# Kernel tuning notes

Hardware: AMD Instinct MI355X
Metric: run time of the kernel (lower is better)

## Reference

```python
import jax, jax.numpy as jnp
import numpy as np

B, T, D, F, E, K, L, S = 8, 1024, 512, 1024, 8, 2, 2, 64
SE, SH = 64, 128  # subject_embed_dim, style_hidden_dim


def setup_inputs() -> dict:
    key = jax.random.key(0)
    ks = jax.random.split(key, 16)
    r = lambda i, shape, s=0.05: (jax.random.normal(ks[i], shape, jnp.float32) * s)
    return dict(
        x=jax.random.normal(ks[0], (B, T, D), jnp.float32),
        subject_ids=jax.random.randint(ks[1], (B,), 0, S),
        # per-layer LayerNorm params (L, D)
        ln_g=jnp.ones((L, D), jnp.float32), ln_b=jnp.zeros((L, D), jnp.float32),
        # per-layer SubjectStyleAlignment params (weights stored (in, out))
        subj_emb=r(2, (L, S, SE), 0.02),
        h1_w=r(3, (L, SE, SH)), h1_b=jnp.zeros((L, SH), jnp.float32),
        h2_w=r(4, (L, SH, SH)), h2_b=jnp.zeros((L, SH), jnp.float32),
        s1_w=r(5, (L, SH, SH // 2)), s1_b=jnp.zeros((L, SH // 2), jnp.float32),
        s2_w=r(6, (L, SH // 2, 2 * D)), s2_b=jnp.zeros((L, 2 * D), jnp.float32),
        # shared TopKRouter: Linear(D, D//2) -> ReLU -> Linear(D//2, E)
        g1_w=r(7, (D, D // 2)), g1_b=jnp.zeros((D // 2,), jnp.float32),
        g2_w=r(8, (D // 2, E)), g2_b=jnp.zeros((E,), jnp.float32),
        # shared ExpertPool of GLU experts (no bias)
        wi0=r(9, (E, D, F)), wi1=r(10, (E, D, F)), wo=r(11, (E, F, D)),
    )


def _layernorm(x, g, b):
    m = x.mean(-1, keepdims=True)
    v = x.var(-1, keepdims=True)  # biased, matches torch LayerNorm
    return (x - m) / jnp.sqrt(v + 1e-5) * g + b


def reference(x, subject_ids, ln_g, ln_b, subj_emb, h1_w, h1_b, h2_w, h2_b,
              s1_w, s1_b, s2_w, s2_b, g1_w, g1_b, g2_w, g2_b, wi0, wi1, wo):
    Bs, Ts, Ds = x.shape
    for l in range(L):  # small fixed layer loop; expert pool + router are shared
        res = x
        h = _layernorm(x, ln_g[l], ln_b[l])
        # SubjectStyleAlignment: instance norm over time axis per (B, D) channel
        mu = h.mean(1, keepdims=True)
        var = h.var(1, keepdims=True)
        hn = (h - mu) / jnp.sqrt(var + 1e-8)
        e = subj_emb[l][subject_ids]                               # (B, SE)
        hh = jax.nn.relu(e @ h1_w[l] + h1_b[l]) @ h2_w[l] + h2_b[l]
        sp = jax.nn.relu(hh @ s1_w[l] + s1_b[l]) @ s2_w[l] + s2_b[l]  # (B, 2D)
        gamma = jax.nn.softplus(sp[:, :Ds]) + 1e-8
        beta = sp[:, Ds:]
        h = hn * gamma[:, None, :] + beta[:, None, :]
        # Router (shared across layers)
        hf = h.reshape(-1, Ds)                                     # (N, D)
        logits = jax.nn.relu(hf @ g1_w + g1_b) @ g2_w + g2_b       # (N, E)
        probs = jax.nn.softmax(logits, -1)
        gates, idx = jax.lax.top_k(probs, K)                       # (N, K)
        gates = gates / (gates.sum(-1, keepdims=True) + 1e-8)
        # combine weights: cw[n, e] = sum_k gates[n,k] * [idx[n,k]==e]
        cw = (jax.nn.one_hot(idx, E, dtype=hf.dtype) * gates[..., None]).sum(1)  # (N, E)
        # GLU experts, computed dense over E then gated-combined
        hid = jax.nn.relu(jnp.einsum('nd,edf->enf', hf, wi0)) \
              * jnp.einsum('nd,edf->enf', hf, wi1)                 # (E, N, F)
        eo = jnp.einsum('enf,efd->end', hid, wo)                   # (E, N, D)
        y = jnp.einsum('ne,end->nd', cw, eo)                       # (N, D)
        x = res + y.reshape(Bs, Ts, Ds)
    return x
```

## Files before the change

kernel.cpp:

```cpp
#include <hip/hip_runtime.h>

typedef unsigned short u16;
typedef unsigned int   u32;
typedef _Float16       f16;
typedef __attribute__((ext_vector_type(8))) _Float16 f16x8;
typedef __attribute__((ext_vector_type(4))) float    f32x4;
typedef __attribute__((ext_vector_type(4))) double   dbl4;

#define NSLOT_ 16384

__device__ __forceinline__ u16 f16bits(f16 h){ union{f16 f; u16 u;} x; x.f = h; return x.u; }

__device__ __forceinline__ void gl_lds16(const void* gptr, void* lptr){
  __builtin_amdgcn_global_load_lds((const __attribute__((address_space(1))) u32*)gptr,
                                   (__attribute__((address_space(3))) u32*)lptr, 16, 0, 0);
}

__device__ __forceinline__ int roff(int row, int lks){
  return ((row >> 1) << 6) + ((lks ^ ((row >> 1) & 3)) << 4) + ((row & 1) << 3);
}

__global__ __launch_bounds__(256) void ln_kernel(const float* __restrict__ x,
    const float* __restrict__ g, const float* __restrict__ bb, float* __restrict__ h){
  int n = blockIdx.x, t = threadIdx.x;
  const float* xr = x + ((size_t)n << 9);
  float2 v = *(const float2*)&xr[t*2];
  double vx = v.x, vy = v.y;
  double s = vx + vy;
  double q = vx*vx + vy*vy;
  #pragma unroll
  for (int o = 32; o > 0; o >>= 1){ s += __shfl_down(s, o, 64); q += __shfl_down(q, o, 64); }
  __shared__ double ls[4], lq_[4];
  __shared__ double sm, sv;
  int wid = t >> 6, lane = t & 63;
  if (lane == 0){ ls[wid] = s; lq_[wid] = q; }
  __syncthreads();
  if (t == 0){
    double S = ls[0]+ls[1]+ls[2]+ls[3], Q = lq_[0]+lq_[1]+lq_[2]+lq_[3];
    double mean = S * (1.0/512.0);
    double var  = Q * (1.0/512.0) - mean*mean;
    sm = mean; sv = 1.0/sqrt(var + 1e-5);
  }
  __syncthreads();
  double mean = sm, inv = sv;
  int d = t*2;
  float2 o;
  o.x = (float)((vx - mean)*inv*(double)g[d]   + (double)bb[d]);
  o.y = (float)((vy - mean)*inv*(double)g[d+1] + (double)bb[d+1]);
  *(float2*)&h[((size_t)n<<9) + d] = o;
}

__global__ __launch_bounds__(256) void colstats(const float* __restrict__ h,
    double* __restrict__ cs, double* __restrict__ cq){
  int bid = blockIdx.x;
  int b = bid >> 3, ch = bid & 7;
  int t = threadIdx.x;
  int col = ch*64 + (t & 63);
  int tp = t >> 6;
  const float* base = h + ((size_t)b << 19);
  double s = 0.0, q = 0.0;
  for (int tt = tp; tt < 1024; tt += 4){
    double v = (double)base[((size_t)tt << 9) + col];
    s += v; q += v*v;
  }
  __shared__ double ls[4][64], lq[4][64];
  ls[tp][t & 63] = s; lq[tp][t & 63] = q;
  __syncthreads();
  if (tp == 0){
    double S = ls[0][t]+ls[1][t]+ls[2][t]+ls[3][t];
    double Q = lq[0][t]+lq[1][t]+lq[2][t]+lq[3][t];
    cs[(b<<9)+col] = S; cq[(b<<9)+col] = Q;
  }
}

__global__ __launch_bounds__(256) void subj_kernel(const int* __restrict__ sid,
    const float* __restrict__ semb,
    const float* __restrict__ h1w, const float* __restrict__ h1b,
    const float* __restrict__ h2w, const float* __restrict__ h2b,
    const float* __restrict__ s1w, const float* __restrict__ s1b,
    const float* __restrict__ s2w, const float* __restrict__ s2b,
    const double* __restrict__ cs, const double* __restrict__ cq,
    double* __restrict__ a64, double* __restrict__ c64, int l){
  __shared__ double ev[64], hid1[128], hh[128], sh[64], sp[1024];
  int t = threadIdx.x;
  int b = blockIdx.x;
  int s = sid[b];
  if (t < 64) ev[t] = (double)semb[l*4096 + s*64 + t];
  __syncthreads();
  if (t < 128){
    double acc = (double)h1b[l*128 + t];
    for (int i = 0; i < 64; ++i) acc += ev[i]*(double)h1w[l*8192 + i*128 + t];
    hid1[t] = acc > 0.0 ? acc : 0.0;
  }
  __syncthreads();
  if (t < 128){
    double acc = (double)h2b[l*128 + t];
    for (int i = 0; i < 128; ++i) acc += hid1[i]*(double)h2w[l*16384 + i*128 + t];
    hh[t] = acc;
  }
  __syncthreads();
  if (t < 64){
    double acc = (double)s1b[l*64 + t];
    for (int i = 0; i < 128; ++i) acc += hh[i]*(double)s1w[l*8192 + i*64 + t];
    sh[t] = acc > 0.0 ? acc : 0.0;
  }
  __syncthreads();
  for (int m = t; m < 1024; m += 256){
    double acc = (double)s2b[l*1024 + m];
    for (int j = 0; j < 64; ++j) acc += sh[j]*(double)s2w[l*65536 + j*1024 + m];
    sp[m] = acc;
  }
  __syncthreads();
  for (int d = t; d < 512; d += 256){
    double mu  = cs[(b<<9)+d] * (1.0/1024.0);
    double var = cq[(b<<9)+d] * (1.0/1024.0) - mu*mu;
    double inv = 1.0/sqrt(var + 1e-8);
    double spv = sp[d];
    double gamma = (spv > 30.0 ? spv : log1p(exp(spv))) + 1e-8;
    double beta  = sp[512 + d];
    double A = gamma * inv;
    a64[(b<<9)+d] = A;
    c64[(b<<9)+d] = beta - mu*A;
  }
}

__global__ __launch_bounds__(256) void hfcast(const float* __restrict__ h,
    const double* __restrict__ a64, const double* __restrict__ c64,
    u16* __restrict__ hfh, u16* __restrict__ hfl){
  size_t i0 = ((size_t)blockIdx.x*256 + threadIdx.x) * 8;
  int n = (int)(i0 >> 9);
  int d0 = (int)(i0 & 511);
  int b = n >> 10;
// ... 109 lines not shown
    #pragma unroll
    for (int e = 0; e < 8; ++e){
      double v = l0[e];
      if (v > b1){ b2 = b1; i2 = i1; b1 = v; i1 = e; }
      else if (v > b2){ b2 = v; i2 = e; }
    }
    double pr1 = p[i1]/s, pr2 = p[i2]/s;
    double den = pr1 + pr2 + 1e-8;
    int n = tok0 + t;
    idxo[2*n] = i1; idxo[2*n+1] = i2;
    wo_[2*n] = (float)(pr1/den); wo_[2*n+1] = (float)(pr2/den);
    atomicAdd(&lcnt[i1], 1); atomicAdd(&lcnt[i2], 1);
  }
  __syncthreads();
  if (t < 8) atomicAdd(&counts[t], lcnt[t]);
}

__global__ void offsets_kernel(const int* __restrict__ counts, int* __restrict__ offs,
                               int* __restrict__ cur){
  if (threadIdx.x == 0 && blockIdx.x == 0){
    int run = 0;
    for (int e = 0; e < 8; ++e){ offs[e] = run; run += counts[e]; cur[e] = 0; }
  }
}

__global__ __launch_bounds__(256) void scatter_kernel(const int* __restrict__ idx,
    const int* __restrict__ offs, int* __restrict__ cur,
    int* __restrict__ tok_of, int* __restrict__ slot_of){
  __shared__ int lcnt[8], lbase[8];
  int t = threadIdx.x;
  int n = blockIdx.x*256 + t;
  if (t < 8) lcnt[t] = 0;
  __syncthreads();
  int e0 = idx[2*n], e1 = idx[2*n+1];
  int p0 = atomicAdd(&lcnt[e0], 1);
  int p1 = atomicAdd(&lcnt[e1], 1);
  __syncthreads();
  if (t < 8) lbase[t] = atomicAdd(&cur[t], lcnt[t]);
  __syncthreads();
  int s0 = offs[e0] + lbase[e0] + p0;
  int s1 = offs[e1] + lbase[e1] + p1;
  tok_of[s0] = n; tok_of[s1] = n;
  slot_of[2*n] = s0; slot_of[2*n+1] = s1;
}

__global__ __launch_bounds__(256) void cvtT16(const float* __restrict__ src,
    u16* __restrict__ dh, u16* __restrict__ dl, int R, int C){
  int bx = blockIdx.x;
  int tilesC = C >> 5, tilesR = R >> 5;
  int e = bx / (tilesR*tilesC);
  int rem = bx % (tilesR*tilesC);
  int rt = rem / tilesC, ct = rem % tilesC;
  __shared__ float tile[32][33];
  int t = threadIdx.x;
  int j = t & 31, i0 = t >> 5;
  const float* s = src + (size_t)e*R*C + (size_t)(rt*32)*C + ct*32;
  for (int ii = i0; ii < 32; ii += 8) tile[ii][j] = s[(size_t)ii*C + j];
  __syncthreads();
  size_t ob = (size_t)e*R*C + (size_t)(ct*32)*R + rt*32;
  for (int ii = i0; ii < 32; ii += 8){
    float v = tile[j][ii];
    f16 hi = (f16)v;
    float rem2 = (v - (float)hi) * 2048.f;
    f16 lo = (f16)rem2;
    dh[ob + (size_t)ii*R + j] = f16bits(hi);
    dl[ob + (size_t)ii*R + j] = f16bits(lo);
  }
}

__global__ __launch_bounds__(256) void up1_kernel(const u16* __restrict__ hfh,
    const u16* __restrict__ hfl,
    const u16* __restrict__ w0h, const u16* __restrict__ w0l,
    const u16* __restrict__ w1h, const u16* __restrict__ w1l,
    const int* __restrict__ tok_of, const int* __restrict__ offs, const int* __restrict__ counts,
    u16* __restrict__ hidh, u16* __restrict__ hidl){
  int bx = blockIdx.x;
  int e  = bx >> 11;
  int mt = (bx >> 4) & 127;
  int nt = bx & 15;
  int base = offs[e], cnt = counts[e];
  int row0 = mt << 7;
  if (row0 >= cnt) return;
  __shared__ __align__(16) u16 Ah[2][4096], Alo[2][4096];
  __shared__ __align__(16) u16 B0h[2][2048], B0l[2][2048], B1h[2][2048], B1l[2][2048];
  int t = threadIdx.x, w = t >> 6, l = t & 63;
  int wm = w >> 1, wn = w & 1;
  int lr = l & 15, lks = l >> 4;
  int riw = ((l >> 3) << 1) | (l & 1);
  int kc16s = ((((l >> 1) & 3) ^ ((l >> 3) & 3)) << 3);
  int ar1 = w*16 + riw;
  int tokA1, tokA2;
  { int ss = base + row0 + ar1;      ss = ss < NSLOT_ ? ss : NSLOT_-1; tokA1 = tok_of[ss]; }
  { int ss = base + row0 + 64 + ar1; ss = ss < NSLOT_ ? ss : NSLOT_-1; tokA2 = tok_of[ss]; }
  const u16* sAh1 = hfh + ((size_t)tokA1 << 9) + kc16s;
  const u16* sAh2 = hfh + ((size_t)tokA2 << 9) + kc16s;
  const u16* sAl1 = hfl + ((size_t)tokA1 << 9) + kc16s;
  const u16* sAl2 = hfl + ((size_t)tokA2 << 9) + kc16s;
  size_t bcol = (size_t)(e*1024 + nt*64);
  size_t bci = (bcol + (size_t)ar1) << 9;
  const u16* sB0h = w0h + bci + kc16s;
  const u16* sB0l = w0l + bci + kc16s;
  const u16* sB1h = w1h + bci + kc16s;
  const u16* sB1l = w1l + bci + kc16s;
  int aoff[4], boff[2];
  #pragma unroll
  for (int mi = 0; mi < 4; ++mi) aoff[mi] = roff(wm*64 + mi*16 + lr, lks);
  #pragma unroll
  for (int ni = 0; ni < 2; ++ni) boff[ni] = roff(wn*32 + ni*16 + lr, lks);
  f32x4 hh0[4][2], cr0[4][2], hh1[4][2], cr1[4][2];
  #pragma unroll
  for (int i = 0; i < 4; ++i)
    #pragma unroll
    for (int j = 0; j < 2; ++j)
      #pragma unroll
      for (int r = 0; r < 4; ++r){ hh0[i][j][r]=0.f; cr0[i][j][r]=0.f; hh1[i][j][r]=0.f; cr1[i][j][r]=0.f; }
#define STG_U(buf, kc) do{ \
    gl_lds16(sAh1 + (kc), &Ah[buf][t*8]); \
    gl_lds16(sAh2 + (kc), &Ah[buf][2048 + t*8]); \
    gl_lds16(sAl1 + (kc), &Alo[buf][t*8]); \
    gl_lds16(sAl2 + (kc), &Alo[buf][2048 + t*8]); \
    gl_lds16(sB0h + (kc), &B0h[buf][t*8]); \
    gl_lds16(sB0l + (kc), &B0l[buf][t*8]); \
    gl_lds16(sB1h + (kc), &B1h[buf][t*8]); \
    gl_lds16(sB1l + (kc), &B1l[buf][t*8]); }while(0)
  STG_U(0, 0);
  for (int ks = 0; ks < 16; ++ks){
    int cur = ks & 1;
    __syncthreads();
    if (ks < 15) STG_U(cur^1, (ks+1)*32);
    f16x8 ah[4], al[4], b0hv[2], b0lv[2], b1hv[2], b1lv[2];
    #pragma unroll
    for (int mi = 0; mi < 4; ++mi){
      ah[mi] = *(const f16x8*)&Ah[cur][aoff[mi]];
      al[mi] = *(const f16x8*)&Alo[cur][aoff[mi]];
    }
    #pragma unroll
    for (int ni = 0; ni < 2; ++ni){
      b0hv[ni] = *(const f16x8*)&B0h[cur][boff[ni]];
      b0lv[ni] = *(const f16x8*)&B0l[cur][boff[ni]];
      b1hv[ni] = *(const f16x8*)&B1h[cur][boff[ni]];
      b1lv[ni] = *(const f16x8*)&B1l[cur][boff[ni]];
    }
    #pragma unroll
    for (int mi = 0; mi < 4; ++mi)
      #pragma unroll
      for (int ni = 0; ni < 2; ++ni){
        hh0[mi][ni] = __builtin_amdgcn_mfma_f32_16x16x32_f16(ah[mi], b0hv[ni], hh0[mi][ni], 0, 0, 0);
        hh1[mi][ni] = __builtin_amdgcn_mfma_f32_16x16x32_f16(ah[mi], b1hv[ni], hh1[mi][ni], 0, 0, 0);
        cr0[mi][ni] = __builtin_amdgcn_mfma_f32_16x16x32_f16(ah[mi], b0lv[ni], cr0[mi][ni], 0, 0, 0);
        cr0[mi][ni] = __builtin_amdgcn_mfma_f32_16x16x32_f16(al[mi], b0hv[ni], cr0[mi][ni], 0, 0, 0);
        cr1[mi][ni] = __builtin_amdgcn_mfma_f32_16x16x32_f16(ah[mi], b1lv[ni], cr1[mi][ni], 0, 0, 0);
        cr1[mi][ni] = __builtin_amdgcn_mfma_f32_16x16x32_f16(al[mi], b1hv[ni], cr1[mi][ni], 0, 0, 0);
      }
  }
#undef STG_U
  #pragma unroll
  for (int mi = 0; mi < 4; ++mi){
    int rb = row0 + wm*64 + mi*16 + lks*4;
    #pragma unroll
    for (int r = 0; r < 4; ++r){
      int rr = rb + r;
      if (rr < cnt){
        size_t orow = ((size_t)(base + rr) << 10) + nt*64;
        #pragma unroll
        for (int ni = 0; ni < 2; ++ni){
          int col = wn*32 + ni*16 + lr;
          float u0 = hh0[mi][ni][r] + cr0[mi][ni][r]*(1.f/2048.f);
          float u1 = hh1[mi][ni][r] + cr1[mi][ni][r]*(1.f/2048.f);
          u0 = u0 > 0.f ? u0 : 0.f;
          float v = u0*u1;
          f16 vh = (f16)v;
          float rem = (v - (float)vh)*2048.f;
          hidh[orow + col] = f16bits(vh);
          hidl[orow + col] = f16bits((f16)rem);
        }
      }
    }
  }
}

__global__ __launch_bounds__(256) void down1_kernel(const u16* __restrict__ hidh,
    const u16* __restrict__ hidl, const u16* __restrict__ wdh, const u16* __restrict__ wdl,
    const int* __restrict__ offs, const int* __restrict__ counts, float* __restrict__ eo){
  int bx = blockIdx.x;
  int e  = bx >> 10;
  int mt = (bx >> 3) & 127;
  int nt = bx & 7;
  int base = offs[e], cnt = counts[e];
  int row0 = mt << 7;
  if (row0 >= cnt) return;
  __shared__ __align__(16) u16 Ah[2][4096], Alo[2][4096];
  __shared__ __align__(16) u16 Bh[2][2048], Bl[2][2048];
  int t = threadIdx.x, w = t >> 6, l = t & 63;
  int wm = w >> 1, wn = w & 1;
  int lr = l & 15, lks = l >> 4;
  int riw = ((l >> 3) << 1) | (l & 1);
  int kc16s = ((((l >> 1) & 3) ^ ((l >> 3) & 3)) << 3);
  int ar1 = w*16 + riw;
  int sA1c = base + row0 + ar1;      sA1c = sA1c < NSLOT_ ? sA1c : NSLOT_-1;
  int sA2c = base + row0 + 64 + ar1; sA2c = sA2c < NSLOT_ ? sA2c : NSLOT_-1;
  const u16* sAh1 = hidh + ((size_t)sA1c << 10) + kc16s;
  const u16* sAh2 = hidh + ((size_t)sA2c << 10) + kc16s;
  const u16* sAl1 = hidl + ((size_t)sA1c << 10) + kc16s;
  const u16* sAl2 = hidl + ((size_t)sA2c << 10) + kc16s;
  size_t bcol = (size_t)(e*512 + nt*64);
  size_t bci = (bcol + (size_t)ar1) << 10;
  const u16* sBh = wdh + bci + kc16s;
  const u16* sBl = wdl + bci + kc16s;
  int aoff[4], boff[2];
  #pragma unroll
  for (int mi = 0; mi < 4; ++mi) aoff[mi] = roff(wm*64 + mi*16 + lr, lks);
  #pragma unroll
  for (int ni = 0; ni < 2; ++ni) boff[ni] = roff(wn*32 + ni*16 + lr, lks);
  f32x4 hh[4][2], cr[4][2];
  #pragma unroll
  for (int i = 0; i < 4; ++i)
    #pragma unroll
    for (int j = 0; j < 2; ++j)
      #pragma unroll
      for (int r = 0; r < 4; ++r){ hh[i][j][r]=0.f; cr[i][j][r]=0.f; }
#define STG_D(buf, kc) do{ \
    gl_lds16(sAh1 + (kc), &Ah[buf][t*8]); \
    gl_lds16(sAh2 + (kc), &Ah[buf][2048 + t*8]); \
    gl_lds16(sAl1 + (kc), &Alo[buf][t*8]); \
    gl_lds16(sAl2 + (kc), &Alo[buf][2048 + t*8]); \
    gl_lds16(sBh + (kc), &Bh[buf][t*8]); \
    gl_lds16(sBl + (kc), &Bl[buf][t*8]); }while(0)
  STG_D(0, 0);
  for (int ks = 0; ks < 32; ++ks){
    int cur = ks & 1;
    __syncthreads();
    if (ks < 31) STG_D(cur^1, (ks+1)*32);
    f16x8 ah[4], al[4], bh[2], bl[2];
    #pragma unroll
    for (int mi = 0; mi < 4; ++mi){
      ah[mi] = *(const f16x8*)&Ah[cur][aoff[mi]];
      al[mi] = *(const f16x8*)&Alo[cur][aoff[mi]];
    }
    #pragma unroll
    for (int ni = 0; ni < 2; ++ni){
      bh[ni] = *(const f16x8*)&Bh[cur][boff[ni]];
      bl[ni] = *(const f16x8*)&Bl[cur][boff[ni]];
    }
    #pragma unroll
    for (int mi = 0; mi < 4; ++mi)
      #pragma unroll
      for (int ni = 0; ni < 2; ++ni){
        hh[mi][ni] = __builtin_amdgcn_mfma_f32_16x16x32_f16(ah[mi], bh[ni], hh[mi][ni], 0, 0, 0);
        cr[mi][ni] = __builtin_amdgcn_mfma_f32_16x16x32_f16(ah[mi], bl[ni], cr[mi][ni], 0, 0, 0);
        cr[mi][ni] = __builtin_amdgcn_mfma_f32_16x16x32_f16(al[mi], bh[ni], cr[mi][ni], 0, 0, 0);
      }
  }
#undef STG_D
  #pragma unroll
  for (int mi = 0; mi < 4; ++mi){
    int rb = row0 + wm*64 + mi*16 + lks*4;
    #pragma unroll
    for (int r = 0; r < 4; ++r){
      int rr = rb + r;
      if (rr < cnt){
        float* orow = eo + (((size_t)(base + rr)) << 9) + nt*64;
        #pragma unroll
        for (int ni = 0; ni < 2; ++ni)
          orow[wn*32 + ni*16 + lr] = hh[mi][ni][r] + cr[mi][ni][r]*(1.f/2048.f);
      }
    }
  }
}

__global__ __launch_bounds__(256) void uph_kernel(const u16* __restrict__ hfh,
    const u16* __restrict__ w0h, const u16* __restrict__ w1h,
    const int* __restrict__ tok_of, const int* __restrict__ offs, const int* __restrict__ counts,
    u16* __restrict__ hidh){
  int bx = blockIdx.x;
  int e  = bx >> 11;
  int mt = (bx >> 4) & 127;
  int nt = bx & 15;
  int base = offs[e], cnt = counts[e];
  int row0 = mt << 7;
  if (row0 >= cnt) return;
  __shared__ __align__(16) u16 Ah[2][4096];
  __shared__ __align__(16) u16 B0h[2][2048], B1h[2][2048];
  int t = threadIdx.x, w = t >> 6, l = t & 63;
  int wm = w >> 1, wn = w & 1;
  int lr = l & 15, lks = l >> 4;
  int riw = ((l >> 3) << 1) | (l & 1);
  int kc16s = ((((l >> 1) & 3) ^ ((l >> 3) & 3)) << 3);
  int ar1 = w*16 + riw;
  int tokA1, tokA2;
  { int ss = base + row0 + ar1;      ss = ss < NSLOT_ ? ss : NSLOT_-1; tokA1 = tok_of[ss]; }
  { int ss = base + row0 + 64 + ar1; ss = ss < NSLOT_ ? ss : NSLOT_-1; tokA2 = tok_of[ss]; }
  const u16* sAh1 = hfh + ((size_t)tokA1 << 9) + kc16s;
  const u16* sAh2 = hfh + ((size_t)tokA2 << 9) + kc16s;
  size_t bcol = (size_t)(e*1024 + nt*64);
  size_t bci = (bcol + (size_t)ar1) << 9;
  const u16* sB0 = w0h + bci + kc16s;
  const u16* sB1 = w1h + bci + kc16s;
  int aoff[4], boff[2];
  #pragma unroll
  for (int mi = 0; mi < 4; ++mi) aoff[mi] = roff(wm*64 + mi*16 + lr, lks);
  #pragma unroll
  for (int ni = 0; ni < 2; ++ni) boff[ni] = roff(wn*32 + ni*16 + lr, lks);
  f32x4 hh0[4][2], hh1[4][2];
  #pragma unroll
  for (int i = 0; i < 4; ++i)
    #pragma unroll
    for (int j = 0; j < 2; ++j)
      #pragma unroll
      for (int r = 0; r < 4; ++r){ hh0[i][j][r]=0.f; hh1[i][j][r]=0.f; }
#define STG_UH(buf, kc) do{ \
    gl_lds16(sAh1 + (kc), &Ah[buf][t*8]); \
    gl_lds16(sAh2 + (kc), &Ah[buf][2048 + t*8]); \
    gl_lds16(sB0 + (kc), &B0h[buf][t*8]); \
    gl_lds16(sB1 + (kc), &B1h[buf][t*8]); }while(0)
  STG_UH(0, 0);
  for (int ks = 0; ks < 16; ++ks){
    int cur = ks & 1;
    __syncthreads();
    if (ks < 15) STG_UH(cur^1, (ks+1)*32);
    f16x8 ah[4], b0v[2], b1v[2];
    #pragma unroll
    for (int mi = 0; mi < 4; ++mi) ah[mi] = *(const f16x8*)&Ah[cur][aoff[mi]];
    #pragma unroll
    for (int ni = 0; ni < 2; ++ni){
      b0v[ni] = *(const f16x8*)&B0h[cur][boff[ni]];
      b1v[ni] = *(const f16x8*)&B1h[cur][boff[ni]];
    }
    #pragma unroll
    for (int mi = 0; mi < 4; ++mi)
      #pragma unroll
      for (int ni = 0; ni < 2; ++ni){
        hh0[mi][ni] = __builtin_amdgcn_mfma_f32_16x16x32_f16(ah[mi], b0v[ni], hh0[mi][ni], 0, 0, 0);
        hh1[mi][ni] = __builtin_amdgcn_mfma_f32_16x16x32_f16(ah[mi], b1v[ni], hh1[mi][ni], 0, 0, 0);
      }
  }
#undef STG_UH
  #pragma unroll
  for (int mi = 0; mi < 4; ++mi){
    int rb = row0 + wm*64 + mi*16 + lks*4;
    #pragma unroll
    for (int r = 0; r < 4; ++r){
      int rr = rb + r;
      if (rr < cnt){
        size_t orow = ((size_t)(base + rr) << 10) + nt*64;
        #pragma unroll
        for (int ni = 0; ni < 2; ++ni){
          int col = wn*32 + ni*16 + lr;
          float u0 = hh0[mi][ni][r];
          u0 = u0 > 0.f ? u0 : 0.f;
          hidh[orow + col] = f16bits((f16)(u0*hh1[mi][ni][r]));
        }
      }
    }
  }
}

__global__ __launch_bounds__(256) void dnh_kernel(const u16* __restrict__ hidh,
    const u16* __restrict__ wdh,
    const int* __restrict__ offs, const int* __restrict__ counts, float* __restrict__ eo){
  int bx = blockIdx.x;
  int e  = bx >> 10;
  int mt = (bx >> 3) & 127;
  int nt = bx & 7;
  int base = offs[e], cnt = counts[e];
  int row0 = mt << 7;
  if (row0 >= cnt) return;
  __shared__ __align__(16) u16 Ah[2][4096];
  __shared__ __align__(16) u16 Bh[2][2048];
  int t = threadIdx.x, w = t >> 6, l = t & 63;
  int wm = w >> 1, wn = w & 1;
  int lr = l & 15, lks = l >> 4;
  int riw = ((l >> 3) << 1) | (l & 1);
  int kc16s = ((((l >> 1) & 3) ^ ((l >> 3) & 3)) << 3);
  int ar1 = w*16 + riw;
  int sA1c = base + row0 + ar1;      sA1c = sA1c < NSLOT_ ? sA1c : NSLOT_-1;
  int sA2c = base + row0 + 64 + ar1; sA2c = sA2c < NSLOT_ ? sA2c : NSLOT_-1;
  const u16* sAh1 = hidh + ((size_t)sA1c << 10) + kc16s;
  const u16* sAh2 = hidh + ((size_t)sA2c << 10) + kc16s;
  size_t bcol = (size_t)(e*512 + nt*64);
  const u16* sB = wdh + ((bcol + (size_t)ar1) << 10) + kc16s;
  int aoff[4], boff[2];
  #pragma unroll
  for (int mi = 0; mi < 4; ++mi) aoff[mi] = roff(wm*64 + mi*16 + lr, lks);
  #pragma unroll
  for (int ni = 0; ni < 2; ++ni) boff[ni] = roff(wn*32 + ni*16 + lr, lks);
  f32x4 hh[4][2];
  #pragma unroll
  for (int i = 0; i < 4; ++i)
    #pragma unroll
    for (int j = 0; j < 2; ++j)
      #pragma unroll
      for (int r = 0; r < 4; ++r) hh[i][j][r] = 0.f;
#define STG_DH(buf, kc) do{ \
    gl_lds16(sAh1 + (kc), &Ah[buf][t*8]); \
    gl_lds16(sAh2 + (kc), &Ah[buf][2048 + t*8]); \
    gl_lds16(sB + (kc), &Bh[buf][t*8]); }while(0)
  STG_DH(0, 0);
  for (int ks = 0; ks < 32; ++ks){
    int cur = ks & 1;
    __syncthreads();
    if (ks < 31) STG_DH(cur^1, (ks+1)*32);
    f16x8 ah[4], bh[2];
    #pragma unroll
    for (int mi = 0; mi < 4; ++mi) ah[mi] = *(const f16x8*)&Ah[cur][aoff[mi]];
    #pragma unroll
    for (int ni = 0; ni < 2; ++ni) bh[ni] = *(const f16x8*)&Bh[cur][boff[ni]];
    #pragma unroll
    for (int mi = 0; mi < 4; ++mi)
      #pragma unroll
      for (int ni = 0; ni < 2; ++ni)
        hh[mi][ni] = __builtin_amdgcn_mfma_f32_16x16x32_f16(ah[mi], bh[ni], hh[mi][ni], 0, 0, 0);
  }
#undef STG_DH
  #pragma unroll
  for (int mi = 0; mi < 4; ++mi){
    int rb = row0 + wm*64 + mi*16 + lks*4;
    #pragma unroll
    for (int r = 0; r < 4; ++r){
      int rr = rb + r;
      if (rr < cnt){
        float* orow = eo + (((size_t)(base + rr)) << 9) + nt*64;
        #pragma unroll
        for (int ni = 0; ni < 2; ++ni)
          orow[wn*32 + ni*16 + lr] = hh[mi][ni][r];
      }
    }
  }
}

__global__ __launch_bounds__(128) void gather_kernel(const float* __restrict__ xin,
    const float* __restrict__ eo, const int* __restrict__ slot_of, const float* __restrict__ wv,
    float* __restrict__ out){
  int n = blockIdx.x, t = threadIdx.x;
  int s0 = slot_of[2*n], s1 = slot_of[2*n+1];
  double w0 = wv[2*n], w1 = wv[2*n+1];
  float4 xi = *(const float4*)&xin[((size_t)n << 9) + t*4];
  float4 e0 = *(const float4*)&eo[((size_t)s0 << 9) + t*4];
  float4 e1 = *(const float4*)&eo[((size_t)s1 << 9) + t*4];
  float4 o;
  o.x = (float)((double)xi.x + w0*(double)e0.x + w1*(double)e1.x);
  o.y = (float)((double)xi.y + w0*(double)e0.y + w1*(double)e1.y);
  o.z = (float)((double)xi.z + w0*(double)e0.z + w1*(double)e1.z);
  o.w = (float)((double)xi.w + w0*(double)e0.w + w1*(double)e1.w);
  *(float4*)&out[((size_t)n << 9) + t*4] = o;
}

extern "C" void kernel_launch(void* const* d_in, const int* in_sizes, int n_in,
                              void* d_out, int out_size, void* d_ws, size_t ws_size,
                              hipStream_t stream) {
  (void)in_sizes; (void)n_in; (void)out_size; (void)ws_size;
  const float* x0   = (const float*)d_in[0];
  const int*   sid  = (const int*)  d_in[1];
  const float* ln_g = (const float*)d_in[2];
  const float* ln_b = (const float*)d_in[3];
  const float* semb = (const float*)d_in[4];
  const float* h1w  = (const float*)d_in[5];
  const float* h1b  = (const float*)d_in[6];
  const float* h2w  = (const float*)d_in[7];
  const float* h2b  = (const float*)d_in[8];
  const float* s1w  = (const float*)d_in[9];
  const float* s1b  = (const float*)d_in[10];
  const float* s2w  = (const float*)d_in[11];
  const float* s2b  = (const float*)d_in[12];
  const float* g1w  = (const float*)d_in[13];
  const float* g1b  = (const float*)d_in[14];
  const float* g2w  = (const float*)d_in[15];
  const float* g2b  = (const float*)d_in[16];
  const float* wi0  = (const float*)d_in[17];
  const float* wi1  = (const float*)d_in[18];
  const float* wo   = (const float*)d_in[19];

  char* W = (char*)d_ws;
  float*  h      = (float*)(W + 0);
  u16*    hfh    = (u16*)  (W + 16777216ULL);
  u16*    hfl    = (u16*)  (W + 25165824ULL);
  float*  eo32   = (float*)(W + 0);
  u16*    hid16h = (u16*)  (W + 33554432ULL);
  u16*    hid16l = (u16*)  (W + 67108864ULL);
  u16*    w0Th   = (u16*)  (W + 100663296ULL);
  u16*    w0Tl   = (u16*)  (W + 109051904ULL);
  u16*    w1Th   = (u16*)  (W + 117440512ULL);
  u16*    w1Tl   = (u16*)  (W + 125829120ULL);
  u16*    woTh   = (u16*)  (W + 134217728ULL);
  u16*    woTl   = (u16*)  (W + 142606336ULL);
  u16*    g1Th   = (u16*)  (W + 150994944ULL);
  u16*    g1Tl   = (u16*)  (W + 151257088ULL);
  double* cs     = (double*)(W + 151519232ULL);
  double* cq     = (double*)(W + 151552000ULL);
  double* a64    = (double*)(W + 151584768ULL);
  double* c64    = (double*)(W + 151617536ULL);
  int*    idxa   = (int*)   (W + 151650304ULL);
  float*  warr   = (float*) (W + 151715840ULL);
  int*    tok_of = (int*)   (W + 151781376ULL);
  int*    slot_of= (int*)   (W + 151846912ULL);
  int*    counts = (int*)   (W + 151912448ULL);
  int*    cur    = counts + 8;
  int*    offs   = counts + 16;

  cvtT16<<<4096, 256, 0, stream>>>(wi0, w0Th, w0Tl, 512, 1024);
  cvtT16<<<4096, 256, 0, stream>>>(wi1, w1Th, w1Tl, 512, 1024);
  cvtT16<<<4096, 256, 0, stream>>>(wo,  woTh, woTl, 1024, 512);
  cvtT16<<<128,  256, 0, stream>>>(g1w, g1Th, g1Tl, 512, 256);

  for (int l = 0; l < 2; ++l){
    const float* xin = l ? (const float*)d_out : x0;
    ln_kernel<<<8192, 256, 0, stream>>>(xin, ln_g + l*512, ln_b + l*512, h);
    colstats<<<64, 256, 0, stream>>>(h, cs, cq);
    subj_kernel<<<8, 256, 0, stream>>>(sid, semb, h1w, h1b, h2w, h2b, s1w, s1b, s2w, s2b,
                                       cs, cq, a64, c64, l);
    hfcast<<<2048, 256, 0, stream>>>(h, a64, c64, hfh, hfl);
    zero_counts<<<1, 64, 0, stream>>>(counts);
    gate2_kernel<<<512, 256, 0, stream>>>(hfh, hfl, g1Th, g1Tl, g1b, g2w, g2b, idxa, warr, counts);
    offsets_kernel<<<1, 1, 0, stream>>>(counts, offs, cur);
    scatter_kernel<<<32, 256, 0, stream>>>(idxa, offs, cur, tok_of, slot_of);
    if (l == 0){
      up1_kernel<<<16384, 256, 0, stream>>>(hfh, hfl, w0Th, w0Tl, w1Th, w1Tl,
                                            tok_of, offs, counts, hid16h, hid16l);
      down1_kernel<<<8192, 256, 0, stream>>>(hid16h, hid16l, woTh, woTl, offs, counts, eo32);
    } else {
      uph_kernel<<<16384, 256, 0, stream>>>(hfh, w0Th, w1Th, tok_of, offs, counts, hid16h);
      dnh_kernel<<<8192, 256, 0, stream>>>(hid16h, woTh, offs, counts, eo32);
    }
    gather_kernel<<<8192, 128, 0, stream>>>(xin, eo32, slot_of, warr, (float*)d_out);
  }
}
```

Measured before the change: 868.7 us.

## Load expert weight fragments directly to registers, fuse gather with next LayerNorm

All four expert GEMM kernels stop staging the B (weight) tiles through LDS. Each lane now loads its weight fragments straight from global memory into registers, with a one-step software prefetch, which cuts LDS traffic and footprint. The layer-1 down-projection widens its N tile to 128 columns and halves its grid. The layer-0 gather is fused with layer-1 LayerNorm, and eo moves to its own workspace region so h stays intact. The risks are uncoalesced global loads for the weights, since each lane reads a different row, and higher register pressure.

```diff
diff --git a/kernel.cpp b/kernel.cpp
--- a/kernel.cpp
+++ b/kernel.cpp
@@ -48,6 +48,49 @@
   o.x = (float)((vx - mean)*inv*(double)g[d]   + (double)bb[d]);
   o.y = (float)((vy - mean)*inv*(double)g[d+1] + (double)bb[d+1]);
   *(float2*)&h[((size_t)n<<9) + d] = o;
+}
+
+__global__ __launch_bounds__(128) void gather_ln(const float* __restrict__ xin,
+    const float* __restrict__ eo, const int* __restrict__ slot_of, const float* __restrict__ wv,
+    const float* __restrict__ g, const float* __restrict__ bb,
+    float* __restrict__ out, float* __restrict__ h){
+  int n = blockIdx.x, t = threadIdx.x;
+  int s0 = slot_of[2*n], s1 = slot_of[2*n+1];
+  double w0 = wv[2*n], w1 = wv[2*n+1];
+  float4 xi = *(const float4*)&xin[((size_t)n << 9) + t*4];
+  float4 e0 = *(const float4*)&eo[((size_t)s0 << 9) + t*4];
+  float4 e1 = *(const float4*)&eo[((size_t)s1 << 9) + t*4];
+  double o0 = (double)xi.x + w0*(double)e0.x + w1*(double)e1.x;
+  double o1 = (double)xi.y + w0*(double)e0.y + w1*(double)e1.y;
+  double o2 = (double)xi.z + w0*(double)e0.z + w1*(double)e1.z;
+  double o3 = (double)xi.w + w0*(double)e0.w + w1*(double)e1.w;
+  float4 o; o.x = (float)o0; o.y = (float)o1; o.z = (float)o2; o.w = (float)o3;
+  *(float4*)&out[((size_t)n << 9) + t*4] = o;
+  double vx = o.x, vy = o.y, vz = o.z, vw = o.w;
+  double s = vx+vy+vz+vw;
+  double q = vx*vx+vy*vy+vz*vz+vw*vw;
+  #pragma unroll
+  for (int off = 32; off > 0; off >>= 1){ s += __shfl_down(s, off, 64); q += __shfl_down(q, off, 64); }
+  __shared__ double ls[2], lq_[2];
+  __shared__ double sm, sv;
+  int wid = t >> 6, lane = t & 63;
+  if (lane == 0){ ls[wid] = s; lq_[wid] = q; }
+  __syncthreads();
+  if (t == 0){
+    double S = ls[0]+ls[1], Q = lq_[0]+lq_[1];
+    double mean = S * (1.0/512.0);
+    double var  = Q * (1.0/512.0) - mean*mean;
+    sm = mean; sv = 1.0/sqrt(var + 1e-5);
+  }
+  __syncthreads();
+  double mean = sm, inv = sv;
+  int d = t*4;
+  float4 ho;
+  ho.x = (float)((vx - mean)*inv*(double)g[d]   + (double)bb[d]);
+  ho.y = (float)((vy - mean)*inv*(double)g[d+1] + (double)bb[d+1]);
+  ho.z = (float)((vz - mean)*inv*(double)g[d+2] + (double)bb[d+2]);
+  ho.w = (float)((vw - mean)*inv*(double)g[d+3] + (double)bb[d+3]);
+  *(float4*)&h[((size_t)n<<9) + d] = ho;
 }
 
 __global__ __launch_bounds__(256) void colstats(const float* __restrict__ h,
@@ -323,7 +366,6 @@
   int row0 = mt << 7;
   if (row0 >= cnt) return;
   __shared__ __align__(16) u16 Ah[2][4096], Alo[2][4096];
-  __shared__ __align__(16) u16 B0h[2][2048], B0l[2][2048], B1h[2][2048], B1l[2][2048];
   int t = threadIdx.x, w = t >> 6, l = t & 63;
   int wm = w >> 1, wn = w & 1;
   int lr = l & 15, lks = l >> 4;
@@ -338,16 +380,18 @@
   const u16* sAl1 = hfl + ((size_t)tokA1 << 9) + kc16s;
   const u16* sAl2 = hfl + ((size_t)tokA2 << 9) + kc16s;
   size_t bcol = (size_t)(e*1024 + nt*64);
-  size_t bci = (bcol + (size_t)ar1) << 9;
-  const u16* sB0h = w0h + bci + kc16s;
-  const u16* sB0l = w0l + bci + kc16s;
-  const u16* sB1h = w1h + bci + kc16s;
-  const u16* sB1l = w1l + bci + kc16s;
-  int aoff[4], boff[2];
+  const u16* pb[8];
+  #pragma unroll
+  for (int ni = 0; ni < 2; ++ni){
+    size_t ci = ((bcol + (size_t)(wn*32 + ni*16 + lr)) << 9) + lks*8;
+    pb[ni]     = w0h + ci;
+    pb[2 + ni] = w0l + ci;
+    pb[4 + ni] = w1h + ci;
+    pb[6 + ni] = w1l + ci;
+  }
+  int aoff[4];
   #pragma unroll
   for (int mi = 0; mi < 4; ++mi) aoff[mi] = roff(wm*64 + mi*16 + lr, lks);
-  #pragma unroll
-  for (int ni = 0; ni < 2; ++ni) boff[ni] = roff(wn*32 + ni*16 + lr, lks);
   f32x4 hh0[4][2], cr0[4][2], hh1[4][2], cr1[4][2];
   #pragma unroll
   for (int i = 0; i < 4; ++i)
@@ -355,46 +399,46 @@
     for (int j = 0; j < 2; ++j)
       #pragma unroll
       for (int r = 0; r < 4; ++r){ hh0[i][j][r]=0.f; cr0[i][j][r]=0.f; hh1[i][j][r]=0.f; cr1[i][j][r]=0.f; }
-#define STG_U(buf, kc) do{ \
+  f16x8 cb[8], nb[8];
+  #pragma unroll
+  for (int i = 0; i < 8; ++i) cb[i] = *(const f16x8*)pb[i];
+#define STG_A(buf, kc) do{ \
     gl_lds16(sAh1 + (kc), &Ah[buf][t*8]); \
     gl_lds16(sAh2 + (kc), &Ah[buf][2048 + t*8]); \
     gl_lds16(sAl1 + (kc), &Alo[buf][t*8]); \
-    gl_lds16(sAl2 + (kc), &Alo[buf][2048 + t*8]); \
-    gl_lds16(sB0h + (kc), &B0h[buf][t*8]); \
-    gl_lds16(sB0l + (kc), &B0l[buf][t*8]); \
-    gl_lds16(sB1h + (kc), &B1h[buf][t*8]); \
-    gl_lds16(sB1l + (kc), &B1l[buf][t*8]); }while(0)
-  STG_U(0, 0);
+    gl_lds16(sAl2 + (kc), &Alo[buf][2048 + t*8]); }while(0)
+  STG_A(0, 0);
   for (int ks = 0; ks < 16; ++ks){
     int cur = ks & 1;
     __syncthreads();
-    if (ks < 15) STG_U(cur^1, (ks+1)*32);
-    f16x8 ah[4], al[4], b0hv[2], b0lv[2], b1hv[2], b1lv[2];
+    if (ks < 15){
+      STG_A(cur^1, (ks+1)*32);
+      #pragma unroll
+      for (int i = 0; i < 8; ++i) nb[i] = *(const f16x8*)(pb[i] + (ks+1)*32);
+    }
+    f16x8 ah[4], al[4];
     #pragma unroll
     for (int mi = 0; mi < 4; ++mi){
       ah[mi] = *(const f16x8*)&Ah[cur][aoff[mi]];
       al[mi] = *(const f16x8*)&Alo[cur][aoff[mi]];
     }
     #pragma unroll
-    for (int ni = 0; ni < 2; ++ni){
-      b0hv[ni] = *(const f16x8*)&B0h[cur][boff[ni]];
-      b0lv[ni] = *(const f16x8*)&B0l[cur][boff[ni]];
-      b1hv[ni] = *(const f16x8*)&B1h[cur][boff[ni]];
-      b1lv[ni] = *(const f16x8*)&B1l[cur][boff[ni]];
-    }
-    #pragma unroll
     for (int mi = 0; mi < 4; ++mi)
       #pragma unroll
       for (int ni = 0; ni < 2; ++ni){
-        hh0[mi][ni] = __builtin_amdgcn_mfma_f32_16x16x32_f16(ah[mi], b0hv[ni], hh0[mi][ni], 0, 0, 0);
-        hh1[mi][ni] = __builtin_amdgcn_mfma_f32_16x16x32_f16(ah[mi], b1hv[ni], hh1[mi][ni], 0, 0, 0);
-        cr0[mi][ni] = __builtin_amdgcn_mfma_f32_16x16x32_f16(ah[mi], b0lv[ni], cr0[mi][ni], 0, 0, 0);
-        cr0[mi][ni] = __builtin_amdgcn_mfma_f32_16x16x32_f16(al[mi], b0hv[ni], cr0[mi][ni], 0, 0, 0);
-        cr1[mi][ni] = __builtin_amdgcn_mfma_f32_16x16x32_f16(ah[mi], b1lv[ni], cr1[mi][ni], 0, 0, 0);
-        cr1[mi][ni] = __builtin_amdgcn_mfma_f32_16x16x32_f16(al[mi], b1hv[ni], cr1[mi][ni], 0, 0, 0);
+        hh0[mi][ni] = __builtin_amdgcn_mfma_f32_16x16x32_f16(ah[mi], cb[ni],     hh0[mi][ni], 0, 0, 0);
+        hh1[mi][ni] = __builtin_amdgcn_mfma_f32_16x16x32_f16(ah[mi], cb[4 + ni], hh1[mi][ni], 0, 0, 0);
+        cr0[mi][ni] = __builtin_amdgcn_mfma_f32_16x16x32_f16(ah[mi], cb[2 + ni], cr0[mi][ni], 0, 0, 0);
+        cr0[mi][ni] = __builtin_amdgcn_mfma_f32_16x16x32_f16(al[mi], cb[ni],     cr0[mi][ni], 0, 0, 0);
+        cr1[mi][ni] = __builtin_amdgcn_mfma_f32_16x16x32_f16(ah[mi], cb[6 + ni], cr1[mi][ni], 0, 0, 0);
+        cr1[mi][ni] = __builtin_amdgcn_mfma_f32_16x16x32_f16(al[mi], cb[4 + ni], cr1[mi][ni], 0, 0, 0);
       }
-  }
-#undef STG_U
+    if (ks < 15){
+      #pragma unroll
+      for (int i = 0; i < 8; ++i) cb[i] = nb[i];
+    }
+  }
+#undef STG_A
   #pragma unroll
   for (int mi = 0; mi < 4; ++mi){
     int rb = row0 + wm*64 + mi*16 + lks*4;
@@ -431,7 +475,6 @@
   int row0 = mt << 7;
   if (row0 >= cnt) return;
   __shared__ __align__(16) u16 Ah[2][4096], Alo[2][4096];
-  __shared__ __align__(16) u16 Bh[2][2048], Bl[2][2048];
   int t = threadIdx.x, w = t >> 6, l = t & 63;
   int wm = w >> 1, wn = w & 1;
   int lr = l & 15, lks = l >> 4;
@@ -445,14 +488,16 @@
   const u16* sAl1 = hidl + ((size_t)sA1c << 10) + kc16s;
   const u16* sAl2 = hidl + ((size_t)sA2c << 10) + kc16s;
   size_t bcol = (size_t)(e*512 + nt*64);
-  size_t bci = (bcol + (size_t)ar1) << 10;
-  const u16* sBh = wdh + bci + kc16s;
-  const u16* sBl = wdl + bci + kc16s;
-  int aoff[4], boff[2];
+  const u16* pb[4];
+  #pragma unroll
+  for (int ni = 0; ni < 2; ++ni){
+    size_t ci = ((bcol + (size_t)(wn*32 + ni*16 + lr)) << 10) + lks*8;
+    pb[ni]     = wdh + ci;
+    pb[2 + ni] = wdl + ci;
+  }
+  int aoff[4];
   #pragma unroll
   for (int mi = 0; mi < 4; ++mi) aoff[mi] = roff(wm*64 + mi*16 + lr, lks);
-  #pragma unroll
-  for (int ni = 0; ni < 2; ++ni) boff[ni] = roff(wn*32 + ni*16 + lr, lks);
   f32x4 hh[4][2], cr[4][2];
   #pragma unroll
   for (int i = 0; i < 4; ++i)
@@ -460,37 +505,41 @@
     for (int j = 0; j < 2; ++j)
       #pragma unroll
       for (int r = 0; r < 4; ++r){ hh[i][j][r]=0.f; cr[i][j][r]=0.f; }
+  f16x8 cb[4], nb[4];
+  #pragma unroll
+  for (int i = 0; i < 4; ++i) cb[i] = *(const f16x8*)pb[i];
 #define STG_D(buf, kc) do{ \
     gl_lds16(sAh1 + (kc), &Ah[buf][t*8]); \
     gl_lds16(sAh2 + (kc), &Ah[buf][2048 + t*8]); \
     gl_lds16(sAl1 + (kc), &Alo[buf][t*8]); \
-    gl_lds16(sAl2 + (kc), &Alo[buf][2048 + t*8]); \
-    gl_lds16(sBh + (kc), &Bh[buf][t*8]); \
-    gl_lds16(sBl + (kc), &Bl[buf][t*8]); }while(0)
+    gl_lds16(sAl2 + (kc), &Alo[buf][2048 + t*8]); }while(0)
   STG_D(0, 0);
   for (int ks = 0; ks < 32; ++ks){
     int cur = ks & 1;
     __syncthreads();
-    if (ks < 31) STG_D(cur^1, (ks+1)*32);
-    f16x8 ah[4], al[4], bh[2], bl[2];
+    if (ks < 31){
+      STG_D(cur^1, (ks+1)*32);
+      #pragma unroll
+      for (int i = 0; i < 4; ++i) nb[i] = *(const f16x8*)(pb[i] + (ks+1)*32);
+    }
+    f16x8 ah[4], al[4];
     #pragma unroll
     for (int mi = 0; mi < 4; ++mi){
       ah[mi] = *(const f16x8*)&Ah[cur][aoff[mi]];
       al[mi] = *(const f16x8*)&Alo[cur][aoff[mi]];
     }
     #pragma unroll
-    for (int ni = 0; ni < 2; ++ni){
-      bh[ni] = *(const f16x8*)&Bh[cur][boff[ni]];
-      bl[ni] = *(const f16x8*)&Bl[cur][boff[ni]];
-    }
-    #pragma unroll
     for (int mi = 0; mi < 4; ++mi)
       #pragma unroll
       for (int ni = 0; ni < 2; ++ni){
-        hh[mi][ni] = __builtin_amdgcn_mfma_f32_16x16x32_f16(ah[mi], bh[ni], hh[mi][ni], 0, 0, 0);
-        cr[mi][ni] = __builtin_amdgcn_mfma_f32_16x16x32_f16(ah[mi], bl[ni], cr[mi][ni], 0, 0, 0);
-        cr[mi][ni] = __builtin_amdgcn_mfma_f32_16x16x32_f16(al[mi], bh[ni], cr[mi][ni], 0, 0, 0);
+        hh[mi][ni] = __builtin_amdgcn_mfma_f32_16x16x32_f16(ah[mi], cb[ni],     hh[mi][ni], 0, 0, 0);
+        cr[mi][ni] = __builtin_amdgcn_mfma_f32_16x16x32_f16(ah[mi], cb[2 + ni], cr[mi][ni], 0, 0, 0);
+        cr[mi][ni] = __builtin_amdgcn_mfma_f32_16x16x32_f16(al[mi], cb[ni],     cr[mi][ni], 0, 0, 0);
       }
+    if (ks < 31){
+      #pragma unroll
+      for (int i = 0; i < 4; ++i) cb[i] = nb[i];
+    }
   }
 #undef STG_D
   #pragma unroll
@@ -521,7 +570,6 @@
   int row0 = mt << 7;
   if (row0 >= cnt) return;
   __shared__ __align__(16) u16 Ah[2][4096];
-  __shared__ __align__(16) u16 B0h[2][2048], B1h[2][2048];
   int t = threadIdx.x, w = t >> 6, l = t & 63;
   int wm = w >> 1, wn = w & 1;
   int lr = l & 15, lks = l >> 4;
@@ -534,14 +582,16 @@
   const u16* sAh1 = hfh + ((size_t)tokA1 << 9) + kc16s;
   const u16* sAh2 = hfh + ((size_t)tokA2 << 9) + kc16s;
   size_t bcol = (size_t)(e*1024 + nt*64);
-  size_t bci = (bcol + (size_t)ar1) << 9;
-  const u16* sB0 = w0h + bci + kc16s;
-  const u16* sB1 = w1h + bci + kc16s;
-  int aoff[4], boff[2];
+  const u16* pb[4];
+  #pragma unroll
+  for (int ni = 0; ni < 2; ++ni){
+    size_t ci = ((bcol + (size_t)(wn*32 + ni*16 + lr)) << 9) + lks*8;
+    pb[ni]     = w0h + ci;
+    pb[2 + ni] = w1h + ci;
+  }
+  int aoff[4];
   #pragma unroll
   for (int mi = 0; mi < 4; ++mi) aoff[mi] = roff(wm*64 + mi*16 + lr, lks);
-  #pragma unroll
-  for (int ni = 0; ni < 2; ++ni) boff[ni] = roff(wn*32 + ni*16 + lr, lks);
   f32x4 hh0[4][2], hh1[4][2];
   #pragma unroll
   for (int i = 0; i < 4; ++i)
@@ -549,31 +599,35 @@
     for (int j = 0; j < 2; ++j)
       #pragma unroll
       for (int r = 0; r < 4; ++r){ hh0[i][j][r]=0.f; hh1[i][j][r]=0.f; }
+  f16x8 cb[4], nb[4];
+  #pragma unroll
+  for (int i = 0; i < 4; ++i) cb[i] = *(const f16x8*)pb[i];
 #define STG_UH(buf, kc) do{ \
     gl_lds16(sAh1 + (kc), &Ah[buf][t*8]); \
-    gl_lds16(sAh2 + (kc), &Ah[buf][2048 + t*8]); \
-    gl_lds16(sB0 + (kc), &B0h[buf][t*8]); \
-    gl_lds16(sB1 + (kc), &B1h[buf][t*8]); }while(0)
+    gl_lds16(sAh2 + (kc), &Ah[buf][2048 + t*8]); }while(0)
   STG_UH(0, 0);
   for (int ks = 0; ks < 16; ++ks){
     int cur = ks & 1;
     __syncthreads();
-    if (ks < 15) STG_UH(cur^1, (ks+1)*32);
-    f16x8 ah[4], b0v[2], b1v[2];
+    if (ks < 15){
+      STG_UH(cur^1, (ks+1)*32);
+      #pragma unroll
+      for (int i = 0; i < 4; ++i) nb[i] = *(const f16x8*)(pb[i] + (ks+1)*32);
+    }
+    f16x8 ah[4];
     #pragma unroll
     for (int mi = 0; mi < 4; ++mi) ah[mi] = *(const f16x8*)&Ah[cur][aoff[mi]];
     #pragma unroll
-    for (int ni = 0; ni < 2; ++ni){
-      b0v[ni] = *(const f16x8*)&B0h[cur][boff[ni]];
-      b1v[ni] = *(const f16x8*)&B1h[cur][boff[ni]];
-    }
-    #pragma unroll
     for (int mi = 0; mi < 4; ++mi)
       #pragma unroll
       for (int ni = 0; ni < 2; ++ni){
-        hh0[mi][ni] = __builtin_amdgcn_mfma_f32_16x16x32_f16(ah[mi], b0v[ni], hh0[mi][ni], 0, 0, 0);
-        hh1[mi][ni] = __builtin_amdgcn_mfma_f32_16x16x32_f16(ah[mi], b1v[ni], hh1[mi][ni], 0, 0, 0);
+        hh0[mi][ni] = __builtin_amdgcn_mfma_f32_16x16x32_f16(ah[mi], cb[ni],     hh0[mi][ni], 0, 0, 0);
+        hh1[mi][ni] = __builtin_amdgcn_mfma_f32_16x16x32_f16(ah[mi], cb[2 + ni], hh1[mi][ni], 0, 0, 0);
       }
+    if (ks < 15){
+      #pragma unroll
+      for (int i = 0; i < 4; ++i) cb[i] = nb[i];
+    }
   }
 #undef STG_UH
   #pragma unroll
@@ -600,14 +654,13 @@
     const u16* __restrict__ wdh,
     const int* __restrict__ offs, const int* __restrict__ counts, float* __restrict__ eo){
   int bx = blockIdx.x;
-  int e  = bx >> 10;
-  int mt = (bx >> 3) & 127;
-  int nt = bx & 7;
+  int e  = bx >> 9;
+  int mt = (bx >> 2) & 127;
+  int nt = bx & 3;
   int base = offs[e], cnt = counts[e];
   int row0 = mt << 7;
   if (row0 >= cnt) return;
   __shared__ __align__(16) u16 Ah[2][4096];
-  __shared__ __align__(16) u16 Bh[2][2048];
   int t = threadIdx.x, w = t >> 6, l = t & 63;
   int wm = w >> 1, wn = w & 1;
   int lr = l & 15, lks = l >> 4;
@@ -618,39 +671,48 @@
   int sA2c = base + row0 + 64 + ar1; sA2c = sA2c < NSLOT_ ? sA2c : NSLOT_-1;
   const u16* sAh1 = hidh + ((size_t)sA1c << 10) + kc16s;
   const u16* sAh2 = hidh + ((size_t)sA2c << 10) + kc16s;
-  size_t bcol = (size_t)(e*512 + nt*64);
-  const u16* sB = wdh + ((bcol + (size_t)ar1) << 10) + kc16s;
-  int aoff[4], boff[2];
+  size_t bcol = (size_t)(e*512 + nt*128);
+  const u16* pb[4];
+  #pragma unroll
+  for (int ni = 0; ni < 4; ++ni)
+    pb[ni] = wdh + ((bcol + (size_t)(wn*64 + ni*16 + lr)) << 10) + lks*8;
+  int aoff[4];
   #pragma unroll
   for (int mi = 0; mi < 4; ++mi) aoff[mi] = roff(wm*64 + mi*16 + lr, lks);
-  #pragma unroll
-  for (int ni = 0; ni < 2; ++ni) boff[ni] = roff(wn*32 + ni*16 + lr, lks);
-  f32x4 hh[4][2];
+  f32x4 hh[4][4];
   #pragma unroll
   for (int i = 0; i < 4; ++i)
     #pragma unroll
-    for (int j = 0; j < 2; ++j)
+    for (int j = 0; j < 4; ++j)
       #pragma unroll
       for (int r = 0; r < 4; ++r) hh[i][j][r] = 0.f;
+  f16x8 cb[4], nb[4];
+  #pragma unroll
+  for (int i = 0; i < 4; ++i) cb[i] = *(const f16x8*)pb[i];
 #define STG_DH(buf, kc) do{ \
     gl_lds16(sAh1 + (kc), &Ah[buf][t*8]); \
-    gl_lds16(sAh2 + (kc), &Ah[buf][2048 + t*8]); \
-    gl_lds16(sB + (kc), &Bh[buf][t*8]); }while(0)
+    gl_lds16(sAh2 + (kc), &Ah[buf][2048 + t*8]); }while(0)
   STG_DH(0, 0);
   for (int ks = 0; ks < 32; ++ks){
     int cur = ks & 1;
     __syncthreads();
-    if (ks < 31) STG_DH(cur^1, (ks+1)*32);
-    f16x8 ah[4], bh[2];
+    if (ks < 31){
+      STG_DH(cur^1, (ks+1)*32);
+      #pragma unroll
+      for (int i = 0; i < 4; ++i) nb[i] = *(const f16x8*)(pb[i] + (ks+1)*32);
+    }
+    f16x8 ah[4];
     #pragma unroll
     for (int mi = 0; mi < 4; ++mi) ah[mi] = *(const f16x8*)&Ah[cur][aoff[mi]];
     #pragma unroll
-    for (int ni = 0; ni < 2; ++ni) bh[ni] = *(const f16x8*)&Bh[cur][boff[ni]];
-    #pragma unroll
     for (int mi = 0; mi < 4; ++mi)
       #pragma unroll
-      for (int ni = 0; ni < 2; ++ni)
-        hh[mi][ni] = __builtin_amdgcn_mfma_f32_16x16x32_f16(ah[mi], bh[ni], hh[mi][ni], 0, 0, 0);
+      for (int ni = 0; ni < 4; ++ni)
+        hh[mi][ni] = __builtin_amdgcn_mfma_f32_16x16x32_f16(ah[mi], cb[ni], hh[mi][ni], 0, 0, 0);
+    if (ks < 31){
+      #pragma unroll
+      for (int i = 0; i < 4; ++i) cb[i] = nb[i];
+    }
   }
 #undef STG_DH
   #pragma unroll
@@ -660,10 +722,10 @@
     for (int r = 0; r < 4; ++r){
       int rr = rb + r;
       if (rr < cnt){
-        float* orow = eo + (((size_t)(base + rr)) << 9) + nt*64;
+        float* orow = eo + (((size_t)(base + rr)) << 9) + nt*128;
         #pragma unroll
-        for (int ni = 0; ni < 2; ++ni)
-          orow[wn*32 + ni*16 + lr] = hh[mi][ni][r];
+        for (int ni = 0; ni < 4; ++ni)
+          orow[wn*64 + ni*16 + lr] = hh[mi][ni][r];
       }
     }
   }
@@ -715,7 +777,7 @@
   float*  h      = (float*)(W + 0);
   u16*    hfh    = (u16*)  (W + 16777216ULL);
   u16*    hfl    = (u16*)  (W + 25165824ULL);
-  float*  eo32   = (float*)(W + 0);
+  float*  eo32   = (float*)(W + 167772160ULL);
   u16*    hid16h = (u16*)  (W + 33554432ULL);
   u16*    hid16l = (u16*)  (W + 67108864ULL);
   u16*    w0Th   = (u16*)  (W + 100663296ULL);
@@ -743,25 +805,29 @@
   cvtT16<<<4096, 256, 0, stream>>>(wo,  woTh, woTl, 1024, 512);
   cvtT16<<<128,  256, 0, stream>>>(g1w, g1Th, g1Tl, 512, 256);
 
-  for (int l = 0; l < 2; ++l){
-    const float* xin = l ? (const float*)d_out : x0;
-    ln_kernel<<<8192, 256, 0, stream>>>(xin, ln_g + l*512, ln_b + l*512, h);
-    colstats<<<64, 256, 0, stream>>>(h, cs, cq);
-    subj_kernel<<<8, 256, 0, stream>>>(sid, semb, h1w, h1b, h2w, h2b, s1w, s1b, s2w, s2b,
-                                       cs, cq, a64, c64, l);
-    hfcast<<<2048, 256, 0, stream>>>(h, a64, c64, hfh, hfl);
-    zero_counts<<<1, 64, 0, stream>>>(counts);
-    gate2_kernel<<<512, 256, 0, stream>>>(hfh, hfl, g1Th, g1Tl, g1b, g2w, g2b, idxa, warr, counts);
-    offsets_kernel<<<1, 1, 0, stream>>>(counts, offs, cur);
-    scatter_kernel<<<32, 256, 0, stream>>>(idxa, offs, cur, tok_of, slot_of);
-    if (l == 0){
-      up1_kernel<<<16384, 256, 0, stream>>>(hfh, hfl, w0Th, w0Tl, w1Th, w1Tl,
-                                            tok_of, offs, counts, hid16h, hid16l);
-      down1_kernel<<<8192, 256, 0, stream>>>(hid16h, hid16l, woTh, woTl, offs, counts, eo32);
-    } else {
-      uph_kernel<<<16384, 256, 0, stream>>>(hfh, w0Th, w1Th, tok_of, offs, counts, hid16h);
-      dnh_kernel<<<8192, 256, 0, stream>>>(hid16h, woTh, offs, counts, eo32);
-    }
-    gather_kernel<<<8192, 128, 0, stream>>>(xin, eo32, slot_of, warr, (float*)d_out);
-  }
-}
+  ln_kernel<<<8192, 256, 0, stream>>>(x0, ln_g, ln_b, h);
+  colstats<<<64, 256, 0, stream>>>(h, cs, cq);
+  subj_kernel<<<8, 256, 0, stream>>>(sid, semb, h1w, h1b, h2w, h2b, s1w, s1b, s2w, s2b,
+                                     cs, cq, a64, c64, 0);
+  hfcast<<<2048, 256, 0, stream>>>(h, a64, c64, hfh, hfl);
+  zero_counts<<<1, 64, 0, stream>>>(counts);
+  gate2_kernel<<<512, 256, 0, stream>>>(hfh, hfl, g1Th, g1Tl, g1b, g2w, g2b, idxa, warr, counts);
+  offsets_kernel<<<1, 1, 0, stream>>>(counts, offs, cur);
+  scatter_kernel<<<32, 256, 0, stream>>>(idxa, offs, cur, tok_of, slot_of);
+  up1_kernel<<<16384, 256, 0, stream>>>(hfh, hfl, w0Th, w0Tl, w1Th, w1Tl,
+                                        tok_of, offs, counts, hid16h, hid16l);
+  down1_kernel<<<8192, 256, 0, stream>>>(hid16h, hid16l, woTh, woTl, offs, counts, eo32);
+  gather_ln<<<8192, 128, 0, stream>>>(x0, eo32, slot_of, warr, ln_g + 512, ln_b + 512,
+                                      (float*)d_out, h);
+  colstats<<<64, 256, 0, stream>>>(h, cs, cq);
+  subj_kernel<<<8, 256, 0, stream>>>(sid, semb, h1w, h1b, h2w, h2b, s1w, s1b, s2w, s2b,
+                                     cs, cq, a64, c64, 1);
+  hfcast<<<2048, 256, 0, stream>>>(h, a64, c64, hfh, hfl);
+  zero_counts<<<1, 64, 0, stream>>>(counts);
+  gate2_kernel<<<512, 256, 0, stream>>>(hfh, hfl, g1Th, g1Tl, g1b, g2w, g2b, idxa, warr, counts);
+  offsets_kernel<<<1, 1, 0, stream>>>(counts, offs, cur);
+  scatter_kernel<<<32, 256, 0, stream>>>(idxa, offs, cur, tok_of, slot_of);
+  uph_kernel<<<16384, 256, 0, stream>>>(hfh, w0Th, w1Th, tok_of, offs, counts, hid16h);
+  dnh_kernel<<<4096, 256, 0, stream>>>(hid16h, woTh, offs, counts, eo32);
+  gather_kernel<<<8192, 128, 0, stream>>>((const float*)d_out, eo32, slot_of, warr, (float*)d_out);
+}
```

New measurement: 1.149 ms. 32.3% more time.
